# Kernel tuning notes

Hardware: AMD Instinct MI355X
Metric: run time of the kernel (lower is better)

## Reference

```python
import jax, jax.numpy as jnp
import numpy as np

B, N, HIST, PRED = 32, 4096, 16, 8
IN_DIM, HID, GCN_OUT, E = 10, 32, 2, 65536


def setup_inputs() -> dict:
    key = jax.random.key(0)
    ks = jax.random.split(key, 11)
    s = 0.15  # keep gate pre-activations in a sane range
    return {
        "pm25_hist": jax.random.normal(ks[0], (B, HIST, N), jnp.float32),
        "feature": jax.random.normal(ks[1], (B, HIST + PRED, N, IN_DIM - 1), jnp.float32),
        "edge_index": jax.random.randint(ks[2], (2, E), 0, N, dtype=jnp.int32),
        "cheb_w": jax.random.normal(ks[3], (2, IN_DIM, GCN_OUT), jnp.float32) * s,
        "cheb_b": jax.random.normal(ks[4], (GCN_OUT,), jnp.float32) * s,
        "x2h_w": jax.random.normal(ks[5], (IN_DIM + GCN_OUT, 4 * HID), jnp.float32) * s,
        "x2h_b": jax.random.normal(ks[6], (4 * HID,), jnp.float32) * s,
        "h2h_w": jax.random.normal(ks[7], (HID, 4 * HID), jnp.float32) * s,
        "h2h_b": jax.random.normal(ks[8], (4 * HID,), jnp.float32) * s,
        "fc_w": jax.random.normal(ks[9], (HID, 1), jnp.float32) * s,
        "fc_b": jax.random.normal(ks[10], (1,), jnp.float32) * s,
    }


def _cheb_norm(edge_index):
    # PyG ChebConv(K=2, sym norm, lambda_max=2): Tx1 = -D^{-1/2} A D^{-1/2} x, zero diagonal
    src, dst = edge_index[0], edge_index[1]
    deg = jnp.zeros((N,), jnp.float32).at[src].add(1.0)
    dis = jnp.where(deg > 0, jax.lax.rsqrt(jnp.maximum(deg, 1e-12)), 0.0)
    return -dis[src] * dis[dst], src, dst


def _cheb_conv(x, src, dst, norm, W, b):
    # x: [B,N,F]; message x[src] aggregated at dst
    msg = x[:, src, :] * norm[None, :, None]
    tx1 = jnp.zeros_like(x[..., :1].repeat(x.shape[-1], -1)).at[:, dst, :].add(msg)
    return jnp.einsum("bnf,fo->bno", x, W[0]) + jnp.einsum("bnf,fo->bno", tx1, W[1]) + b


def _lstm(x, h, c, x2h_w, x2h_b, h2h_w, h2h_b):
    g = x @ x2h_w + x2h_b + h @ h2h_w + h2h_b  # [B,N,4H]
    i, f, gc, o = jnp.split(g, 4, axis=-1)
    c = jax.nn.sigmoid(f) * c + jax.nn.sigmoid(i) * jnp.tanh(gc)
    h = jax.nn.sigmoid(o) * jnp.tanh(c)
    return h, c


def reference(pm25_hist, feature, edge_index, cheb_w, cheb_b, x2h_w, x2h_b, h2h_w, h2h_b, fc_w, fc_b):
    norm, src, dst = _cheb_norm(edge_index)

    def step(carry, x):
        h, c = carry
        xg = jax.nn.sigmoid(_cheb_conv(x, src, dst, norm, cheb_w, cheb_b))
        h, c = _lstm(jnp.concatenate([x, xg], -1), h, c, x2h_w, x2h_b, h2h_w, h2h_b)
        return (h, c), None

    h = jnp.zeros((B, N, HID), jnp.float32)
    c = jnp.zeros((B, N, HID), jnp.float32)

    # history phase
    xs_hist = jnp.concatenate([pm25_hist[..., None], feature[:, :HIST]], -1)  # [B,HIST,N,10]
    (h, c), _ = jax.lax.scan(step, (h, c), jnp.swapaxes(xs_hist, 0, 1))
    xn = h @ fc_w + fc_b  # [B,N,1]

    # prediction phase (recurrent through xn)
    def pred_step(carry, feat_t):
        h, c, xn = carry
        x = jnp.concatenate([xn, feat_t], -1)  # [B,N,10]
        (h, c), _ = step((h, c), x)
        xn = h @ fc_w + fc_b
        return (h, c, xn), xn

    _, ys = jax.lax.scan(pred_step, (h, c, xn), jnp.swapaxes(feature[:, HIST:], 0, 1))
    return jnp.squeeze(jnp.swapaxes(ys, 0, 1), -1)  # [B,PRED,N]
```

## Files before the change

### kernel.cpp

```cpp
#include <hip/hip_runtime.h>
#include <math.h>

#define Bb    32
#define Nn    4096
#define HISTC 16
#define PREDC 8
#define TTC   24
#define EC    65536
#define BN    (Bb*Nn)
#define NSL   768

typedef float f32x2 __attribute__((ext_vector_type(2)));
typedef float f32x4 __attribute__((ext_vector_type(4)));
typedef __fp16 f16x8 __attribute__((ext_vector_type(8)));
typedef __fp16 fp16v2 __attribute__((ext_vector_type(2)));

__device__ __forceinline__ float sigm_f(float x){
  return __builtin_amdgcn_rcpf(1.f + __expf(-x));
}
__device__ __forceinline__ float tanh_f(float x){
  return fmaf(-2.f, __builtin_amdgcn_rcpf(1.f + __expf(2.f*x)), 1.f);
}
__device__ __forceinline__ unsigned pk2(float a, float b){
  fp16v2 v = __builtin_amdgcn_cvt_pkrtz(a, b);
  return __builtin_bit_cast(unsigned, v);
}
__device__ __forceinline__ void unpk2(unsigned u, float& a, float& b){
  fp16v2 v = __builtin_bit_cast(fp16v2, u);
  a = (float)v.x; b = (float)v.y;
}
__device__ __forceinline__ f32x4 mfma16(uint4 a, uint4 b, f32x4 c){
  return __builtin_amdgcn_mfma_f32_16x16x32_f16(
      __builtin_bit_cast(f16x8, a), __builtin_bit_cast(f16x8, b), c, 0, 0, 0);
}

__global__ void k_deg(const int* __restrict__ ei, int* deg, int* cnt){
  int e = blockIdx.x*blockDim.x + threadIdx.x;
  if (e < EC){ atomicAdd(&deg[ei[e]],1); atomicAdd(&cnt[ei[EC+e]],1); }
}
__global__ void k_scan(const int* __restrict__ cnt, int* ptr){
  __shared__ int sd[1024];
  int t = threadIdx.x;
  int c0=cnt[4*t], c1=cnt[4*t+1], c2=cnt[4*t+2], c3=cnt[4*t+3];
  int s = c0+c1+c2+c3;
  sd[t] = s; __syncthreads();
  for (int off=1; off<1024; off<<=1){
    int v = (t>=off) ? sd[t-off] : 0;
    __syncthreads();
    sd[t] += v;
    __syncthreads();
  }
  int excl = sd[t]-s;
  ptr[4*t]=excl; ptr[4*t+1]=excl+c0; ptr[4*t+2]=excl+c0+c1; ptr[4*t+3]=excl+c0+c1+c2;
  if (t==1023) ptr[4096]=sd[1023];
}
__global__ void k_misc(const int* __restrict__ deg, float* __restrict__ dis,
                       const float* __restrict__ x2hw, const float* __restrict__ h2hw,
                       const float* __restrict__ x2hb, const float* __restrict__ h2hb,
                       _Float16* __restrict__ wfrag){
  if (blockIdx.x == 0){
    #pragma unroll
    for (int k=0;k<4;++k){
      int n = threadIdx.x + k*1024;
      dis[n] = deg[n] > 0 ? rsqrtf((float)deg[n]) : 0.f;
    }
  } else {
    int i = (blockIdx.x-1)*1024 + threadIdx.x;
    int f = i >> 9, lane = (i >> 3) & 63, j = i & 7;
    int kt = f >> 3, ct = f & 7;
    int k = kt*32 + (lane>>4)*8 + j;
    int col = ct*16 + (lane&15);
    float v;
    if (k < 12)       v = x2hw[k*128 + col];
    else if (k == 12) v = x2hb[col] + h2hb[col];
    else if (k < 32)  v = 0.f;
    else              v = h2hw[(k-32)*128 + col];
    wfrag[f*512 + lane*8 + j] = (_Float16)v;
  }
}
__global__ void k_fill(const int* __restrict__ ei, const float* __restrict__ dis,
                       const int* __restrict__ ptr, int* fillc, int2* __restrict__ epack){
  int e = blockIdx.x*blockDim.x + threadIdx.x;
  if (e < EC){
    int s = ei[e], d = ei[EC+e];
    int pos = ptr[d] + atomicAdd(&fillc[d],1);
    epack[pos] = make_int2(s, __float_as_int(-dis[s]*dis[d]));
  }
}

__global__ __launch_bounds__(256)
void k_zt(const float* __restrict__ pm25, const float* __restrict__ feat,
          const float* __restrict__ cw, f32x2* __restrict__ zT){
  __shared__ f32x2 tile[64][65];
  int nb = blockIdx.x & 63, sb = blockIdx.x >> 6;
  int n0 = nb*64, s0 = sb*64;
  int tid = threadIdx.x;
  #pragma unroll
  for (int k=0;k<16;++k){
    int i = tid + k*256;
    int r = i >> 6, c = i & 63;
    int slice = s0 + r, n = n0 + c;
    int b = slice & 31;
    int t;
    float z0, z1;
    if (slice < 512){
      t = (slice >> 5) & 15;
      float x0 = pm25[((size_t)(b*HISTC + t))*Nn + n];
      z0 = x0*cw[20]; z1 = x0*cw[21];
    } else {
      t = HISTC + ((slice - 512) >> 5);
      z0 = 0.f; z1 = 0.f;
    }
    const float* fp = feat + ((size_t)(b*TTC + t)*Nn + n)*9;
    #pragma unroll
    for (int f=0;f<9;++f){
      float v = fp[f];
      z0 = fmaf(v, cw[20+(f+1)*2+0], z0); z1 = fmaf(v, cw[20+(f+1)*2+1], z1);
    }
    tile[r][c] = (f32x2){z0, z1};
  }
  __syncthreads();
  #pragma unroll
  for (int k=0;k<16;++k){
    int i = tid + k*256;
    int r = i >> 6, c = i & 63;
    zT[(size_t)(n0 + r)*NSL + s0 + c] = tile[c][r];
  }
}

__global__ __launch_bounds__(256)
void k_tr(const f32x2* __restrict__ in, f32x2* __restrict__ out, int R, int C){
  __shared__ f32x2 tile[64][65];
  int tilesR = R >> 6;
  int br = blockIdx.x % tilesR, bc = blockIdx.x / tilesR;
  int r0 = br << 6, c0 = bc << 6;
  for (int i=threadIdx.x; i<4096; i+=256){
    int r = i>>6, c = i&63;
    tile[r][c] = in[(size_t)(r0+r)*C + c0+c];
  }
  __syncthreads();
  for (int i=threadIdx.x; i<4096; i+=256){
    int r = i>>6, c = i&63;
    out[(size_t)(c0+r)*R + r0+c] = tile[c][r];
  }
}

__global__ __launch_bounds__(64)
void k_aggc(const int* __restrict__ ptr, const int2* __restrict__ epack,
            const float4* __restrict__ zT, float4* __restrict__ aggT){
  int n  = blockIdx.x & (Nn-1);
  int cb = blockIdx.x >> 12;
  int col = cb*64 + threadIdx.x;
  int p0 = ptr[n], p1 = ptr[n+1];
  f32x4 acc = {0.f,0.f,0.f,0.f};
  int i = p0;
  for (; i+1 < p1; i += 2){
    int2 e0 = epack[i], e1 = epack[i+1];
    float w0 = __int_as_float(e0.y), w1 = __int_as_float(e1.y);
    float4 z0 = zT[(size_t)e0.x*384 + col];
    float4 z1 = zT[(size_t)e1.x*384 + col];
    acc.x = fmaf(w0, z0.x, acc.x); acc.y = fmaf(w0, z0.y, acc.y);
    acc.z = fmaf(w0, z0.z, acc.z); acc.w = fmaf(w0, z0.w, acc.w);
    acc.x = fmaf(w1, z1.x, acc.x); acc.y = fmaf(w1, z1.y, acc.y);
    acc.z = fmaf(w1, z1.z, acc.z); acc.w = fmaf(w1, z1.w, acc.w);
  }
  if (i < p1){
    int2 e = epack[i];
    float w = __int_as_float(e.y);
    float4 z = zT[(size_t)e.x*384 + col];
    acc.x = fmaf(w, z.x, acc.x); acc.y = fmaf(w, z.y, acc.y);
    acc.z = fmaf(w, z.z, acc.z); acc.w = fmaf(w, z.w, acc.w);
  }
  aggT[(size_t)n*384 + col] = make_float4(acc.x, acc.y, acc.z, acc.w);
}

#define POINTWISE(r)                                                            \
  c0[r] = fmaf(sigm_f(acc[0][r]), tanh_f(acc[4][r]), sigm_f(acc[2][r])*c0[r]);  \
  h0[r] = sigm_f(acc[6][r])*tanh_f(c0[r]);                                      \
  c1[r] = fmaf(sigm_f(acc[1][r]), tanh_f(acc[5][r]), sigm_f(acc[3][r])*c1[r]);  \
  h1[r] = sigm_f(acc[7][r])*tanh_f(c1[r]);

__global__ __launch_bounds__(256,1)
void k_hist(const float* __restrict__ pm25, const float* __restrict__ feat,
            const f32x2* __restrict__ aggH,
            const float* __restrict__ cw, const float* __restrict__ cb,
            const uint4* __restrict__ wfrag,
            const float* __restrict__ fcw, const float* __restrict__ fcb,
            uint4* __restrict__ hfragO, uint4* __restrict__ cO,
            float* __restrict__ xn0){
  __shared__ __align__(16) uint4 wl[1024];
  __shared__ __align__(16) _Float16 hl[4][16][40];
  int tid = threadIdx.x;
  int lane = tid & 63, w = tid >> 6;
  for (int i = tid; i < 1024; i += 256) wl[i] = wfrag[i];
  int gw = blockIdx.x*4 + w;
  int r0 = gw*16;
  int b = r0 >> 12, n0 = r0 & (Nn-1);
  int l15 = lane & 15, g4 = lane >> 4;
  int nrow = n0 + l15;
  const float* pb = pm25 + (size_t)b*HISTC*Nn + nrow;
  const float* fb = feat + ((size_t)b*TTC*Nn + nrow)*9;

  float fw0 = fcw[l15], fw1 = fcw[l15+16];
  const f32x4 zacc = {0.f,0.f,0.f,0.f};

  uint4 ah = make_uint4(0,0,0,0);
  float c0[4]={0,0,0,0}, c1[4]={0,0,0,0};
  float h0[4], h1[4];
  __syncthreads();

  #pragma unroll 1
  for (int t=0; t<HISTC; ++t){
    int wofs = lane;
    asm volatile("" : "+v"(wofs));
    const float* fbt = fb + (size_t)t*Nn*9;
    float xv[9]; float a0 = 0.f, a1 = 0.f; float x0 = 0.f;
    if (g4 == 0){
      x0 = pb[(size_t)t*Nn];
      #pragma unroll
      for (int f=0;f<7;++f) xv[f] = fbt[f];
      a0 = x0*cw[0]; a1 = x0*cw[1];
      #pragma unroll
      for (int f=0;f<7;++f){ a0 += xv[f]*cw[(f+1)*2]; a1 += xv[f]*cw[(f+1)*2+1]; }
    } else if (g4 == 1){
      xv[7] = fbt[7]; xv[8] = fbt[8];
      a0 = cb[0] + xv[7]*cw[16] + xv[8]*cw[18];
      a1 = cb[1] + xv[7]*cw[17] + xv[8]*cw[19];
    } else if (g4 == 2){
      f32x2 ag = aggH[((size_t)(t*Bb + b))*Nn + nrow];
      a0 = ag.x; a1 = ag.y;
    }
    a0 += __shfl_xor(a0, 16); a0 += __shfl_xor(a0, 32);
    a1 += __shfl_xor(a1, 16); a1 += __shfl_xor(a1, 32);
    float xg0 = sigm_f(a0), xg1 = sigm_f(a1);

    uint4 ax;
    if (g4 == 0){
      ax.x = pk2(x0, xv[0]);     ax.y = pk2(xv[1], xv[2]);
      ax.z = pk2(xv[3], xv[4]);  ax.w = pk2(xv[5], xv[6]);
    } else if (g4 == 1){
      ax.x = pk2(xv[7], xv[8]);  ax.y = pk2(xg0, xg1);
      ax.z = pk2(1.f, 0.f);      ax.w = 0u;
    } else {
      ax = make_uint4(0,0,0,0);
    }

    f32x4 acc[8];
    #pragma unroll
    for (int ct=0; ct<8; ++ct){
      uint4 b0 = wl[wofs + ct*64];
      uint4 b1 = wl[wofs + 512 + ct*64];
      acc[ct] = mfma16(ax, b0, zacc);
      acc[ct] = mfma16(ah, b1, acc[ct]);
    }

    POINTWISE(0) POINTWISE(1) POINTWISE(2) POINTWISE(3)

    #pragma unroll
    for (int r=0;r<4;++r){
      hl[w][g4*4+r][l15]    = (_Float16)h0[r];
      hl[w][g4*4+r][l15+16] = (_Float16)h1[r];
    }
    asm volatile("s_waitcnt lgkmcnt(0)" ::: "memory");
    ah = *(const uint4*)&hl[w][l15][g4*8];
  }

  hfragO[(size_t)gw*64 + lane] = ah;
  {
    uint4 cp;
    cp.x = pk2(c0[0], c0[1]); cp.y = pk2(c0[2], c0[3]);
    cp.z = pk2(c1[0], c1[1]); cp.w = pk2(c1[2], c1[3]);
    cO[(size_t)gw*64 + lane] = cp;
  }
  #pragma unroll
  for (int r=0;r<4;++r){
    float p = fmaf(h0[r], fw0, h1[r]*fw1);
    p += __shfl_xor(p, 1, 16); p += __shfl_xor(p, 2, 16);
    p += __shfl_xor(p, 4, 16); p += __shfl_xor(p, 8, 16);
    if (l15 == 0) xn0[r0 + g4*4 + r] = p + fcb[0];
  }
}

__global__ __launch_bounds__(256,1)
void k_pred_cell(const float* __restrict__ feat,
                 const float* __restrict__ xnI, float* __restrict__ xnO,
                 const f32x2* __restrict__ aggzf,
                 const int* __restrict__ ptr, const int2* __restrict__ epack,
                 const float* __restrict__ cw, const float* __restrict__ cb,
                 const uint4* __restrict__ wfrag,
                 const float* __restrict__ fcw, const float* __restrict__ fcb,
                 uint4* __restrict__ hfrag, uint4* __restrict__ cS,
                 float* __restrict__ out, int t){
  __shared__ __align__(16) uint4 wl[1024];
  __shared__ __align__(16) _Float16 hl[4][16][40];
  int tid = threadIdx.x;
  int lane = tid & 63, w = tid >> 6;
  for (int i = tid; i < 1024; i += 256) wl[i] = wfrag[i];
  int gw = blockIdx.x*4 + w;
  int r0 = gw*16;
  int b = r0 >> 12, n0 = r0 & (Nn-1);
  int l15 = lane & 15, g4 = lane >> 4;
  int nrow = n0 + l15;

  float fw0 = fcw[l15], fw1 = fcw[l15+16];

  uint4 ah = hfrag[(size_t)gw*64 + lane];
  float c0[4], c1[4];
  {
    uint4 cv = cS[(size_t)gw*64 + lane];
    unpk2(cv.x, c0[0], c0[1]); unpk2(cv.y, c0[2], c0[3]);
    unpk2(cv.z, c1[0], c1[1]); unpk2(cv.w, c1[2], c1[3]);
  }
  float h0[4], h1[4];
  const f32x4 zacc = {0.f,0.f,0.f,0.f};

  const float* fbt = feat + ((size_t)(b*TTC + t)*Nn + nrow)*9;
  const float* xb = xnI + (size_t)b*Nn;
  float xv[9]; float a0 = 0.f, a1 = 0.f; float x0 = 0.f;
  if (g4 == 0){
    x0 = xb[nrow];
    #pragma unroll
    for (int f=0;f<7;++f) xv[f] = fbt[f];
    a0 = x0*cw[0]; a1 = x0*cw[1];
    #pragma unroll
    for (int f=0;f<7;++f){ a0 += xv[f]*cw[(f+1)*2]; a1 += xv[f]*cw[(f+1)*2+1]; }
  } else if (g4 == 1){
    xv[7] = fbt[7]; xv[8] = fbt[8];
    a0 = cb[0] + xv[7]*cw[16] + xv[8]*cw[18];
    a1 = cb[1] + xv[7]*cw[17] + xv[8]*cw[19];
  } else if (g4 == 2){
    f32x2 azf = aggzf[(size_t)b*Nn + nrow];
    a0 = azf.x; a1 = azf.y;
  }
  {
    int p0 = ptr[nrow], p1 = ptr[nrow+1];
    float pax = 0.f;
    for (int i = p0 + g4; i < p1; i += 4){
      int2 e = epack[i];
      pax = fmaf(__int_as_float(e.y), xb[e.x], pax);
    }
    a0 = fmaf(pax, cw[20], a0);
    a1 = fmaf(pax, cw[21], a1);
  }
  a0 += __shfl_xor(a0, 16); a0 += __shfl_xor(a0, 32);
  a1 += __shfl_xor(a1, 16); a1 += __shfl_xor(a1, 32);
  float xg0 = sigm_f(a0), xg1 = sigm_f(a1);

  uint4 ax;
  if (g4 == 0){
    ax.x = pk2(x0, xv[0]);     ax.y = pk2(xv[1], xv[2]);
    ax.z = pk2(xv[3], xv[4]);  ax.w = pk2(xv[5], xv[6]);
  } else if (g4 == 1){
    ax.x = pk2(xv[7], xv[8]);  ax.y = pk2(xg0, xg1);
    ax.z = pk2(1.f, 0.f);      ax.w = 0u;
  } else {
    ax = make_uint4(0,0,0,0);
  }

  __syncthreads();
  f32x4 acc[8];
  #pragma unroll
  for (int ct=0; ct<8; ++ct){
    uint4 b0 = wl[lane + ct*64];
    uint4 b1 = wl[lane + 512 + ct*64];
    acc[ct] = mfma16(ax, b0, zacc);
    acc[ct] = mfma16(ah, b1, acc[ct]);
  }

  POINTWISE(0) POINTWISE(1) POINTWISE(2) POINTWISE(3)

  #pragma unroll
  for (int r=0;r<4;++r){
    hl[w][g4*4+r][l15]    = (_Float16)h0[r];
    hl[w][g4*4+r][l15+16] = (_Float16)h1[r];
  }
  asm volatile("s_waitcnt lgkmcnt(0)" ::: "memory");
  ah = *(const uint4*)&hl[w][l15][g4*8];

  hfrag[(size_t)gw*64 + lane] = ah;
  {
    uint4 cp;
    cp.x = pk2(c0[0], c0[1]); cp.y = pk2(c0[2], c0[3]);
    cp.z = pk2(c1[0], c1[1]); cp.w = pk2(c1[2], c1[3]);
    cS[(size_t)gw*64 + lane] = cp;
  }
  #pragma unroll
  for (int r=0;r<4;++r){
    float p = fmaf(h0[r], fw0, h1[r]*fw1);
    p += __shfl_xor(p, 1, 16); p += __shfl_xor(p, 2, 16);
    p += __shfl_xor(p, 4, 16); p += __shfl_xor(p, 8, 16);
    if (l15 == 0){
      float rr = p + fcb[0];
      int nr = n0 + g4*4 + r;
      xnO[r0 + g4*4 + r] = rr;
      out[(size_t)b*PREDC*Nn + nr] = rr;
    }
  }
}

extern "C" void kernel_launch(void* const* d_in, const int* in_sizes, int n_in,
                              void* d_out, int out_size, void* d_ws, size_t ws_size,
                              hipStream_t stream){
  const float* pm25 = (const float*)d_in[0];
  const float* feat = (const float*)d_in[1];
  const int*   ei   = (const int*)d_in[2];
  const float* cw   = (const float*)d_in[3];
  const float* cb   = (const float*)d_in[4];
  const float* x2hw = (const float*)d_in[5];
  const float* x2hb = (const float*)d_in[6];
  const float* h2hw = (const float*)d_in[7];
  const float* h2hb = (const float*)d_in[8];
  const float* fcw  = (const float*)d_in[9];
  const float* fcb  = (const float*)d_in[10];
  float* out = (float*)d_out;

  char* wsp = (char*)d_ws;
  size_t off = 0;
  auto take = [&](size_t bytes)->char*{
    char* r = wsp + off; off += (bytes + 255) & ~(size_t)255; return r;
  };
  int*      deg   = (int*)      take(Nn*4);
  int*      cnt   = (int*)      take(Nn*4);
  int*      fillc = (int*)      take(Nn*4);
  int*      ptr   = (int*)      take((Nn+1)*4);
  float*    dis   = (float*)    take(Nn*4);
  int2*     epack = (int2*)     take(EC*8);
  _Float16* wfrag = (_Float16*) take(16*512*2);
  char*     bufA  =             take((size_t)NSL*Nn*8);
  char*     bufB  =             take((size_t)NSL*Nn*8);
  float*    xn0   = (float*)    take((size_t)BN*4);
  float*    xn1   = (float*)    take((size_t)BN*4);

  uint4*  hfrag = (uint4*)bufA;
  uint4*  cbuf  = (uint4*)(bufA + (size_t)8388608);

  (void)hipMemsetAsync(deg, 0, Nn*4*3, stream);

  k_deg <<<EC/256, 256, 0, stream>>>(ei, deg, cnt);
  k_scan<<<1, 1024, 0, stream>>>(cnt, ptr);
  k_misc<<<9, 1024, 0, stream>>>(deg, dis, x2hw, h2hw, x2hb, h2hb, wfrag);
  k_fill<<<EC/256, 256, 0, stream>>>(ei, dis, ptr, fillc, epack);

  k_zt<<<(NSL/64)*(Nn/64), 256, 0, stream>>>(pm25, feat, cw, (f32x2*)bufB);
  k_aggc<<<6*Nn, 64, 0, stream>>>(ptr, epack, (const float4*)bufB, (float4*)bufA);
  k_tr<<<(Nn/64)*(NSL/64), 256, 0, stream>>>((const f32x2*)bufA, (f32x2*)bufB, Nn, NSL);

  const f32x2* aggAll = (const f32x2*)bufB;

  k_hist<<<BN/64, 256, 0, stream>>>(pm25, feat, aggAll, cw, cb,
                                    (const uint4*)wfrag, fcw, fcb,
                                    hfrag, cbuf, xn0);

  for (int tp = 0; tp < PREDC; ++tp){
    int t = HISTC + tp;
    const float* xi = (tp & 1) ? xn1 : xn0;
    float*       xo = (tp & 1) ? xn0 : xn1;
    k_pred_cell<<<BN/64, 256, 0, stream>>>(feat, xi, xo,
                                           aggAll + (size_t)(512 + tp*Bb)*Nn,
                                           ptr, epack, cw, cb,
                                           (const uint4*)wfrag, fcw, fcb,
                                           hfrag, cbuf, out + (size_t)tp*Nn, t);
  }
}
```

Measured before the change: 373.6 us.

## Fuse prediction-phase timesteps into one persistent cooperative kernel with grid sync

Replaces the eight per-timestep prediction kernel launches with a single cooperative kernel of 512 blocks. Each wave keeps four row tiles' h and c state in registers across all steps, and a grid-wide sync between steps handles the xn dependency. This removes launch gaps and the per-step global round trips of h and c state. In exchange, each wave does four tiles of work serially, grid.sync adds its own cost, and running two blocks per CU may raise register pressure. If the cooperative launch fails, the code falls back to the per-step kernels.

```diff
diff --git a/kernel.cpp b/kernel.cpp
--- a/kernel.cpp
+++ b/kernel.cpp
@@ -1,5 +1,8 @@
 #include <hip/hip_runtime.h>
+#include <hip/hip_cooperative_groups.h>
 #include <math.h>
+
+namespace cg = cooperative_groups;
 
 #define Bb    32
 #define Nn    4096
@@ -281,16 +284,165 @@
   }
 }
 
+#define PRED_CELL_BODY(AH, C0, C1, XNI, XNO, AGGZF, TSTEP, TPW_OUT_TP)          \
+  {                                                                             \
+    const float* fbt = feat + ((size_t)(b*TTC + (TSTEP))*Nn + nrow)*9;          \
+    const float* xb = (XNI) + (size_t)b*Nn;                                     \
+    float xv[9]; float a0 = 0.f, a1 = 0.f; float x0 = 0.f;                      \
+    if (g4 == 0){                                                               \
+      x0 = xb[nrow];                                                            \
+      _Pragma("unroll")                                                         \
+      for (int f=0;f<7;++f) xv[f] = fbt[f];                                     \
+      a0 = x0*cw[0]; a1 = x0*cw[1];                                             \
+      _Pragma("unroll")                                                         \
+      for (int f=0;f<7;++f){ a0 += xv[f]*cw[(f+1)*2]; a1 += xv[f]*cw[(f+1)*2+1]; }\
+    } else if (g4 == 1){                                                        \
+      xv[7] = fbt[7]; xv[8] = fbt[8];                                           \
+      a0 = cb[0] + xv[7]*cw[16] + xv[8]*cw[18];                                 \
+      a1 = cb[1] + xv[7]*cw[17] + xv[8]*cw[19];                                 \
+    } else if (g4 == 2){                                                        \
+      f32x2 azf = (AGGZF)[(size_t)b*Nn + nrow];                                 \
+      a0 = azf.x; a1 = azf.y;                                                   \
+    }                                                                           \
+    {                                                                           \
+      int p0 = ptr[nrow], p1 = ptr[nrow+1];                                     \
+      float pax = 0.f;                                                          \
+      for (int i = p0 + g4; i < p1; i += 4){                                    \
+        int2 e = epack[i];                                                      \
+        pax = fmaf(__int_as_float(e.y), xb[e.x], pax);                          \
+      }                                                                         \
+      a0 = fmaf(pax, cw[20], a0);                                               \
+      a1 = fmaf(pax, cw[21], a1);                                               \
+    }                                                                           \
+    a0 += __shfl_xor(a0, 16); a0 += __shfl_xor(a0, 32);                         \
+    a1 += __shfl_xor(a1, 16); a1 += __shfl_xor(a1, 32);                         \
+    float xg0 = sigm_f(a0), xg1 = sigm_f(a1);                                   \
+    uint4 ax;                                                                   \
+    if (g4 == 0){                                                               \
+      ax.x = pk2(x0, xv[0]);     ax.y = pk2(xv[1], xv[2]);                      \
+      ax.z = pk2(xv[3], xv[4]);  ax.w = pk2(xv[5], xv[6]);                      \
+    } else if (g4 == 1){                                                        \
+      ax.x = pk2(xv[7], xv[8]);  ax.y = pk2(xg0, xg1);                          \
+      ax.z = pk2(1.f, 0.f);      ax.w = 0u;                                     \
+    } else {                                                                    \
+      ax = make_uint4(0,0,0,0);                                                 \
+    }                                                                           \
+    f32x4 acc[8];                                                               \
+    _Pragma("unroll")                                                           \
+    for (int ct=0; ct<8; ++ct){                                                 \
+      uint4 b0 = wl[lane + ct*64];                                              \
+      uint4 b1 = wl[lane + 512 + ct*64];                                        \
+      acc[ct] = mfma16(ax, b0, zacc);                                           \
+      acc[ct] = mfma16((AH), b1, acc[ct]);                                      \
+    }                                                                           \
+    float h0[4], h1[4];                                                         \
+    float (&c0)[4] = (C0); float (&c1)[4] = (C1);                               \
+    POINTWISE(0) POINTWISE(1) POINTWISE(2) POINTWISE(3)                         \
+    _Pragma("unroll")                                                           \
+    for (int r=0;r<4;++r){                                                      \
+      hl[w][g4*4+r][l15]    = (_Float16)h0[r];                                  \
+      hl[w][g4*4+r][l15+16] = (_Float16)h1[r];                                  \
+    }                                                                           \
+    asm volatile("s_waitcnt lgkmcnt(0)" ::: "memory");                          \
+    (AH) = *(const uint4*)&hl[w][l15][g4*8];                                    \
+    _Pragma("unroll")                                                           \
+    for (int r=0;r<4;++r){                                                      \
+      float p = fmaf(h0[r], fw0, h1[r]*fw1);                                    \
+      p += __shfl_xor(p, 1, 16); p += __shfl_xor(p, 2, 16);                     \
+      p += __shfl_xor(p, 4, 16); p += __shfl_xor(p, 8, 16);                     \
+      if (l15 == 0){                                                            \
+        float rr = p + fcb[0];                                                  \
+        int nr = n0 + g4*4 + r;                                                 \
+        (XNO)[r0 + g4*4 + r] = rr;                                              \
+        out[((size_t)b*PREDC + (TPW_OUT_TP))*Nn + nr] = rr;                     \
+      }                                                                         \
+    }                                                                           \
+  }
+
+__global__ __launch_bounds__(256,2)
+void k_pred_all(const float* __restrict__ feat,
+                float* __restrict__ xnA, float* __restrict__ xnB,
+                const f32x2* __restrict__ aggAll,
+                const int* __restrict__ ptr, const int2* __restrict__ epack,
+                const float* __restrict__ cw, const float* __restrict__ cb,
+                const uint4* __restrict__ wfrag,
+                const float* __restrict__ fcw, const float* __restrict__ fcb,
+                const uint4* __restrict__ hfragI, const uint4* __restrict__ cI,
+                float* __restrict__ out){
+  cg::grid_group gg = cg::this_grid();
+  __shared__ __align__(16) uint4 wl[1024];
+  __shared__ __align__(16) _Float16 hl[4][16][40];
+  int tid = threadIdx.x;
+  int lane = tid & 63, w = tid >> 6;
+  for (int i = tid; i < 1024; i += 256) wl[i] = wfrag[i];
+  int gw0 = blockIdx.x*4 + w;
+  int l15 = lane & 15, g4 = lane >> 4;
+  float fw0 = fcw[l15], fw1 = fcw[l15+16];
+  const f32x4 zacc = {0.f,0.f,0.f,0.f};
+
+  uint4 ah0, ah1, ah2, ah3;
+  float c0s0[4], c1s0[4], c0s1[4], c1s1[4], c0s2[4], c1s2[4], c0s3[4], c1s3[4];
+  {
+    uint4 cv;
+    ah0 = hfragI[(size_t)(gw0         )*64 + lane];
+    cv  = cI[(size_t)(gw0)*64 + lane];
+    unpk2(cv.x, c0s0[0], c0s0[1]); unpk2(cv.y, c0s0[2], c0s0[3]);
+    unpk2(cv.z, c1s0[0], c1s0[1]); unpk2(cv.w, c1s0[2], c1s0[3]);
+    ah1 = hfragI[(size_t)(gw0 + 2048)*64 + lane];
+    cv  = cI[(size_t)(gw0 + 2048)*64 + lane];
+    unpk2(cv.x, c0s1[0], c0s1[1]); unpk2(cv.y, c0s1[2], c0s1[3]);
+    unpk2(cv.z, c1s1[0], c1s1[1]); unpk2(cv.w, c1s1[2], c1s1[3]);
+    ah2 = hfragI[(size_t)(gw0 + 4096)*64 + lane];
+    cv  = cI[(size_t)(gw0 + 4096)*64 + lane];
+    unpk2(cv.x, c0s2[0], c0s2[1]); unpk2(cv.y, c0s2[2], c0s2[3]);
+    unpk2(cv.z, c1s2[0], c1s2[1]); unpk2(cv.w, c1s2[2], c1s2[3]);
+    ah3 = hfragI[(size_t)(gw0 + 6144)*64 + lane];
+    cv  = cI[(size_t)(gw0 + 6144)*64 + lane];
+    unpk2(cv.x, c0s3[0], c0s3[1]); unpk2(cv.y, c0s3[2], c0s3[3]);
+    unpk2(cv.z, c1s3[0], c1s3[1]); unpk2(cv.w, c1s3[2], c1s3[3]);
+  }
+  __syncthreads();
+
+  #pragma unroll 1
+  for (int tp=0; tp<PREDC; ++tp){
+    const float* xnI = (tp & 1) ? xnB : xnA;
+    float*       xnO = (tp & 1) ? xnA : xnB;
+    const f32x2* aggzf = aggAll + (size_t)(512 + tp*Bb)*Nn;
+    int t = HISTC + tp;
+    {
+      int gw = gw0;
+      int r0 = gw*16; int b = r0 >> 12, n0 = r0 & (Nn-1); int nrow = n0 + l15;
+      PRED_CELL_BODY(ah0, c0s0, c1s0, xnI, xnO, aggzf, t, tp)
+    }
+    {
+      int gw = gw0 + 2048;
+      int r0 = gw*16; int b = r0 >> 12, n0 = r0 & (Nn-1); int nrow = n0 + l15;
+      PRED_CELL_BODY(ah1, c0s1, c1s1, xnI, xnO, aggzf, t, tp)
+    }
+    {
+      int gw = gw0 + 4096;
+      int r0 = gw*16; int b = r0 >> 12, n0 = r0 & (Nn-1); int nrow = n0 + l15;
+      PRED_CELL_BODY(ah2, c0s2, c1s2, xnI, xnO, aggzf, t, tp)
+    }
+    {
+      int gw = gw0 + 6144;
+      int r0 = gw*16; int b = r0 >> 12, n0 = r0 & (Nn-1); int nrow = n0 + l15;
+      PRED_CELL_BODY(ah3, c0s3, c1s3, xnI, xnO, aggzf, t, tp)
+    }
+    if (tp < PREDC-1) gg.sync();
+  }
+}
+
 __global__ __launch_bounds__(256,1)
 void k_pred_cell(const float* __restrict__ feat,
-                 const float* __restrict__ xnI, float* __restrict__ xnO,
+                 const float* __restrict__ xnI, float* __restrict__ xnO_,
                  const f32x2* __restrict__ aggzf,
                  const int* __restrict__ ptr, const int2* __restrict__ epack,
                  const float* __restrict__ cw, const float* __restrict__ cb,
                  const uint4* __restrict__ wfrag,
                  const float* __restrict__ fcw, const float* __restrict__ fcb,
                  uint4* __restrict__ hfrag, uint4* __restrict__ cS,
-                 float* __restrict__ out, int t){
+                 float* __restrict__ out, int t, int tp){
   __shared__ __align__(16) uint4 wl[1024];
   __shared__ __align__(16) _Float16 hl[4][16][40];
   int tid = threadIdx.x;
@@ -301,100 +453,27 @@
   int b = r0 >> 12, n0 = r0 & (Nn-1);
   int l15 = lane & 15, g4 = lane >> 4;
   int nrow = n0 + l15;
-
   float fw0 = fcw[l15], fw1 = fcw[l15+16];
+  const f32x4 zacc = {0.f,0.f,0.f,0.f};
 
   uint4 ah = hfrag[(size_t)gw*64 + lane];
-  float c0[4], c1[4];
+  float c0v[4], c1v[4];
   {
     uint4 cv = cS[(size_t)gw*64 + lane];
-    unpk2(cv.x, c0[0], c0[1]); unpk2(cv.y, c0[2], c0[3]);
-    unpk2(cv.z, c1[0], c1[1]); unpk2(cv.w, c1[2], c1[3]);
-  }
-  float h0[4], h1[4];
-  const f32x4 zacc = {0.f,0.f,0.f,0.f};
-
-  const float* fbt = feat + ((size_t)(b*TTC + t)*Nn + nrow)*9;
-  const float* xb = xnI + (size_t)b*Nn;
-  float xv[9]; float a0 = 0.f, a1 = 0.f; float x0 = 0.f;
-  if (g4 == 0){
-    x0 = xb[nrow];
-    #pragma unroll
-    for (int f=0;f<7;++f) xv[f] = fbt[f];
-    a0 = x0*cw[0]; a1 = x0*cw[1];
-    #pragma unroll
-    for (int f=0;f<7;++f){ a0 += xv[f]*cw[(f+1)*2]; a1 += xv[f]*cw[(f+1)*2+1]; }
-  } else if (g4 == 1){
-    xv[7] = fbt[7]; xv[8] = fbt[8];
-    a0 = cb[0] + xv[7]*cw[16] + xv[8]*cw[18];
-    a1 = cb[1] + xv[7]*cw[17] + xv[8]*cw[19];
-  } else if (g4 == 2){
-    f32x2 azf = aggzf[(size_t)b*Nn + nrow];
-    a0 = azf.x; a1 = azf.y;
-  }
-  {
-    int p0 = ptr[nrow], p1 = ptr[nrow+1];
-    float pax = 0.f;
-    for (int i = p0 + g4; i < p1; i += 4){
-      int2 e = epack[i];
-      pax = fmaf(__int_as_float(e.y), xb[e.x], pax);
-    }
-    a0 = fmaf(pax, cw[20], a0);
-    a1 = fmaf(pax, cw[21], a1);
-  }
-  a0 += __shfl_xor(a0, 16); a0 += __shfl_xor(a0, 32);
-  a1 += __shfl_xor(a1, 16); a1 += __shfl_xor(a1, 32);
-  float xg0 = sigm_f(a0), xg1 = sigm_f(a1);
-
-  uint4 ax;
-  if (g4 == 0){
-    ax.x = pk2(x0, xv[0]);     ax.y = pk2(xv[1], xv[2]);
-    ax.z = pk2(xv[3], xv[4]);  ax.w = pk2(xv[5], xv[6]);
-  } else if (g4 == 1){
-    ax.x = pk2(xv[7], xv[8]);  ax.y = pk2(xg0, xg1);
-    ax.z = pk2(1.f, 0.f);      ax.w = 0u;
-  } else {
-    ax = make_uint4(0,0,0,0);
-  }
-
+    unpk2(cv.x, c0v[0], c0v[1]); unpk2(cv.y, c0v[2], c0v[3]);
+    unpk2(cv.z, c1v[0], c1v[1]); unpk2(cv.w, c1v[2], c1v[3]);
+  }
   __syncthreads();
-  f32x4 acc[8];
-  #pragma unroll
-  for (int ct=0; ct<8; ++ct){
-    uint4 b0 = wl[lane + ct*64];
-    uint4 b1 = wl[lane + 512 + ct*64];
-    acc[ct] = mfma16(ax, b0, zacc);
-    acc[ct] = mfma16(ah, b1, acc[ct]);
-  }
-
-  POINTWISE(0) POINTWISE(1) POINTWISE(2) POINTWISE(3)
-
-  #pragma unroll
-  for (int r=0;r<4;++r){
-    hl[w][g4*4+r][l15]    = (_Float16)h0[r];
-    hl[w][g4*4+r][l15+16] = (_Float16)h1[r];
-  }
-  asm volatile("s_waitcnt lgkmcnt(0)" ::: "memory");
-  ah = *(const uint4*)&hl[w][l15][g4*8];
+
+  float* xnO = xnO_;
+  PRED_CELL_BODY(ah, c0v, c1v, xnI, xnO, aggzf - (size_t)0, t, tp)
 
   hfrag[(size_t)gw*64 + lane] = ah;
   {
     uint4 cp;
-    cp.x = pk2(c0[0], c0[1]); cp.y = pk2(c0[2], c0[3]);
-    cp.z = pk2(c1[0], c1[1]); cp.w = pk2(c1[2], c1[3]);
+    cp.x = pk2(c0v[0], c0v[1]); cp.y = pk2(c0v[2], c0v[3]);
+    cp.z = pk2(c1v[0], c1v[1]); cp.w = pk2(c1v[2], c1v[3]);
     cS[(size_t)gw*64 + lane] = cp;
-  }
-  #pragma unroll
-  for (int r=0;r<4;++r){
-    float p = fmaf(h0[r], fw0, h1[r]*fw1);
-    p += __shfl_xor(p, 1, 16); p += __shfl_xor(p, 2, 16);
-    p += __shfl_xor(p, 4, 16); p += __shfl_xor(p, 8, 16);
-    if (l15 == 0){
-      float rr = p + fcb[0];
-      int nr = n0 + g4*4 + r;
-      xnO[r0 + g4*4 + r] = rr;
-      out[(size_t)b*PREDC*Nn + nr] = rr;
-    }
   }
 }
 
@@ -451,14 +530,30 @@
                                     (const uint4*)wfrag, fcw, fcb,
                                     hfrag, cbuf, xn0);
 
-  for (int tp = 0; tp < PREDC; ++tp){
-    int t = HISTC + tp;
-    const float* xi = (tp & 1) ? xn1 : xn0;
-    float*       xo = (tp & 1) ? xn0 : xn1;
-    k_pred_cell<<<BN/64, 256, 0, stream>>>(feat, xi, xo,
-                                           aggAll + (size_t)(512 + tp*Bb)*Nn,
-                                           ptr, epack, cw, cb,
-                                           (const uint4*)wfrag, fcw, fcb,
-                                           hfrag, cbuf, out + (size_t)tp*Nn, t);
-  }
-}
+  hipError_t cerr;
+  {
+    const uint4* wfp = (const uint4*)wfrag;
+    const uint4* hfp = hfrag;
+    const uint4* cbp = cbuf;
+    void* args[] = {
+      (void*)&feat, (void*)&xn0, (void*)&xn1, (void*)&aggAll,
+      (void*)&ptr, (void*)&epack, (void*)&cw, (void*)&cb,
+      (void*)&wfp, (void*)&fcw, (void*)&fcb,
+      (void*)&hfp, (void*)&cbp, (void*)&out
+    };
+    cerr = hipLaunchCooperativeKernel((void*)k_pred_all, dim3(512), dim3(256),
+                                      args, 0, stream);
+  }
+  if (cerr != hipSuccess){
+    for (int tp = 0; tp < PREDC; ++tp){
+      int t = HISTC + tp;
+      const float* xi = (tp & 1) ? xn1 : xn0;
+      float*       xo = (tp & 1) ? xn0 : xn1;
+      k_pred_cell<<<BN/64, 256, 0, stream>>>(feat, xi, xo,
+                                             aggAll + (size_t)(512 + tp*Bb)*Nn,
+                                             ptr, epack, cw, cb,
+                                             (const uint4*)wfrag, fcw, fcb,
+                                             hfrag, cbuf, out, t, tp);
+    }
+  }
+}
```

Result: slower. 784.0 us (+109.9%).
